# Performance work log

Hardware: AMD Instinct MI355X
Metric: run time of the kernel (lower is better)

## Reference

```python
import jax, jax.numpy as jnp
import numpy as np

HIDDEN = 1280
NUM_HEADS = 16
HEAD_DIM = HIDDEN // NUM_HEADS  # 80
ROPE_DIM = HEAD_DIM // 2        # 40
THETA = 10000.0
SEQ = 3072


def setup_inputs() -> dict:
    key = jax.random.key(0)
    ks = jax.random.split(key, 6)
    hidden_states = jax.random.normal(ks[0], (SEQ, HIDDEN), dtype=jnp.float32)
    position_ids = jax.random.randint(ks[1], (SEQ, 2), 0, 64, dtype=jnp.int32)
    qkv_w = jax.random.normal(ks[2], (HIDDEN, 3 * HIDDEN), dtype=jnp.float32) * (HIDDEN ** -0.5)
    qkv_b = jax.random.normal(ks[3], (3 * HIDDEN,), dtype=jnp.float32) * 0.02
    o_w = jax.random.normal(ks[4], (HIDDEN, HIDDEN), dtype=jnp.float32) * (HIDDEN ** -0.5)
    o_b = jax.random.normal(ks[5], (HIDDEN,), dtype=jnp.float32) * 0.02
    return {"hidden_states": hidden_states, "position_ids": position_ids,
            "qkv_w": qkv_w, "qkv_b": qkv_b, "o_w": o_w, "o_b": o_b}


def _rotate_half(x):
    x1, x2 = jnp.split(x, 2, axis=-1)
    return jnp.concatenate([-x2, x1], axis=-1)


def reference(hidden_states, position_ids, qkv_w, qkv_b, o_w, o_b):
    seq_len = hidden_states.shape[0]
    # fused QKV projection
    qkv = hidden_states @ qkv_w + qkv_b                     # (S, 3*H*D)
    qkv = qkv.reshape(seq_len, 3, NUM_HEADS, HEAD_DIM)
    q, k, v = qkv[:, 0], qkv[:, 1], qkv[:, 2]               # each (S, h, d)
    # 2D RoPE: inv_freq over rope dim = head_dim // 2
    inv_freq = 1.0 / (THETA ** (jnp.arange(0, ROPE_DIM, 2, dtype=jnp.float32) / ROPE_DIM))
    pos = position_ids.astype(jnp.float32)
    h_freqs = jnp.outer(pos[:, 0], inv_freq)                # (S, rope/2)
    w_freqs = jnp.outer(pos[:, 1], inv_freq)                # (S, rope/2)
    freqs = jnp.concatenate([h_freqs, w_freqs], axis=-1)    # (S, rope)
    emb = jnp.concatenate([freqs, freqs], axis=-1)          # (S, head_dim)
    cos = jnp.cos(emb)[:, None, :]                          # (S, 1, d)
    sin = jnp.sin(emb)[:, None, :]
    q = q * cos + _rotate_half(q) * sin
    k = k * cos + _rotate_half(k) * sin
    # manual attention
    scaling = HEAD_DIM ** -0.5
    attn = jnp.einsum('qhd,khd->hqk', q * scaling, k)       # (h, S, S)
    attn = jax.nn.softmax(attn, axis=-1)
    out = jnp.einsum('hqk,khd->qhd', attn, v)               # (S, h, d)
    out = out.reshape(seq_len, HIDDEN)
    return out @ o_w + o_b
```

## Files before the change

### kernel.cpp

```cpp
#include <hip/hip_runtime.h>

#define SEQ  3072
#define HID  1280
#define NH   16
#define HD   80
#define NQKV 3840
#define KSP  2

typedef unsigned short u16;
typedef unsigned int u32;
typedef __attribute__((ext_vector_type(8))) short short8;
typedef __attribute__((ext_vector_type(4))) short short4v;
typedef __attribute__((ext_vector_type(4))) float floatx4;

__device__ __forceinline__ u16 f2bf(float x) {
    u32 u = __float_as_uint(x);
    u += 0x7fffu + ((u >> 16) & 1u);
    return (u16)(u >> 16);
}
__device__ __forceinline__ u32 packrne(float a, float b) {
    return (u32)f2bf(a) | ((u32)f2bf(b) << 16);
}

typedef const __attribute__((address_space(1))) unsigned int* gp1_t;
typedef __attribute__((address_space(3))) unsigned int* lp3_t;
__device__ __forceinline__ void gld16(const void* g, void* l) {
    __builtin_amdgcn_global_load_lds((gp1_t)g, (lp3_t)l, 16, 0, 0);
}

__device__ __forceinline__ int swz80(int c, int r) {
    return (c < 8) ? (c ^ (r & 7)) : (8 + ((c - 8) ^ ((r >> 2) & 1)));
}

__global__ void prep_k(const int* __restrict__ pos, float* __restrict__ cosb,
                       float* __restrict__ sinb, const float* __restrict__ hs,
                       u16* __restrict__ hH, const float* __restrict__ qkvw,
                       u16* __restrict__ wT, const float* __restrict__ ow,
                       u16* __restrict__ owT) {
    __shared__ float tile[32][33];
    const int b = blockIdx.x, t = threadIdx.x;
    if (b < 480) {
        int i = b * 256 + t;
        int s = i / 40, j = i % 40;
        float p = (float)((j < 20) ? pos[s * 2] : pos[s * 2 + 1]);
        int k = (j < 20) ? j : j - 20;
        float inv = powf(10000.0f, -(float)k / 20.0f);
        float a = p * inv;
        cosb[s * 40 + j] = cosf(a);
        sinb[s * 40 + j] = sinf(a);
    } else if (b < 4320) {
        int i = (b - 480) * 256 + t;
        const float4 x = ((const float4*)hs)[i];
        uint2 o;
        o.x = packrne(x.x, x.y);
        o.y = packrne(x.z, x.w);
        ((uint2*)hH)[i] = o;
    } else {
        const float* w;
        u16* dst;
        int K, N, nx, ky;
        if (b < 9120) {
            int i = b - 4320;
            nx = i % 120; ky = i / 120; w = qkvw; dst = wT; K = HID; N = NQKV;
        } else {
            int i = b - 9120;
            nx = i % 40; ky = i / 40; w = ow; dst = owT; K = HID; N = HID;
        }
        int n0 = nx * 32, k0 = ky * 32;
        int c = t & 31, r8 = t >> 5;
        for (int rr = r8; rr < 32; rr += 8)
            tile[rr][c] = w[(size_t)(k0 + rr) * N + n0 + c];
        __syncthreads();
        for (int rr = r8; rr < 32; rr += 8)
            dst[(size_t)(n0 + rr) * K + k0 + c] = f2bf(tile[c][rr]);
    }
}

__global__ __launch_bounds__(256, 3) void gemm_bf16_k(
    const u16* __restrict__ A, const u16* __restrict__ B,
    const float* __restrict__ bias, float* __restrict__ C,
    int M, int N, int K, int mode) {
    __shared__ u16 lA[128 * 64], lB[128 * 64];
    const int t = threadIdx.x, lane = t & 63, w = t >> 6;
    const int qi = lane & 15, quad = lane >> 4;
    int id = blockIdx.x;
    int xcd = id & 7, sN = id >> 3;
    int m_idx, n_idx;
    if (mode == 0) {
        n_idx = (xcd & 1) * 15 + sN % 15;
        m_idx = (xcd >> 1) * 6 + sN / 15;
    } else {
        m_idx = xcd * 3 + sN / 10;
        n_idx = sN % 10;
    }
    const int m0 = m_idx * 128, n0 = n_idx * 128;
    const int wm = (w >> 1) * 64, wn = (w & 1) * 64;

    floatx4 acc[4][4];
    for (int mi = 0; mi < 4; mi++)
        for (int ni = 0; ni < 4; ni++) acc[mi][ni] = (floatx4){0.f, 0.f, 0.f, 0.f};

    const int rg = lane >> 3;
    const int ce = ((lane & 7) ^ rg) * 8;
    size_t gA[4], gB[4];
    for (int g = 0; g < 4; g++) {
        int row = w * 32 + g * 8 + rg;
        gA[g] = (size_t)(m0 + row) * K + ce;
        gB[g] = (size_t)(n0 + row) * K + ce;
    }

    for (int k0 = 0; k0 < K; k0 += 64) {
        for (int g = 0; g < 4; g++) {
            gld16(A + gA[g] + k0, &lA[(w * 32 + g * 8) * 64]);
            gld16(B + gB[g] + k0, &lB[(w * 32 + g * 8) * 64]);
        }
        __syncthreads();
        short8 af[4][2], bf[4][2];
        for (int mi = 0; mi < 4; mi++) {
            int row = wm + mi * 16 + qi;
            for (int kh = 0; kh < 2; kh++)
                af[mi][kh] = *(const short8*)&lA[row * 64 + (((kh * 4 + quad) ^ (row & 7)) << 3)];
        }
        for (int ni = 0; ni < 4; ni++) {
            int row = wn + ni * 16 + qi;
            for (int kh = 0; kh < 2; kh++)
                bf[ni][kh] = *(const short8*)&lB[row * 64 + (((kh * 4 + quad) ^ (row & 7)) << 3)];
        }
        for (int mi = 0; mi < 4; mi++)
            for (int ni = 0; ni < 4; ni++) {
                acc[mi][ni] = __builtin_amdgcn_mfma_f32_16x16x32_bf16(af[mi][0], bf[ni][0], acc[mi][ni], 0, 0, 0);
                acc[mi][ni] = __builtin_amdgcn_mfma_f32_16x16x32_bf16(af[mi][1], bf[ni][1], acc[mi][ni], 0, 0, 0);
            }
        __syncthreads();
    }
    for (int mi = 0; mi < 4; mi++)
        for (int ni = 0; ni < 4; ni++) {
            int col = n0 + wn + ni * 16 + qi;
            int rowb = m0 + wm + mi * 16 + quad * 4;
            float b = bias[col];
            for (int r = 0; r < 4; r++)
                C[(size_t)(rowb + r) * N + col] = acc[mi][ni][r] + b;
        }
}

__global__ void pack_qkv_k(const float* __restrict__ qkv, const float* __restrict__ cosb,
                           const float* __restrict__ sinb,
                           u16* __restrict__ Qs, u16* __restrict__ Ks, u16* __restrict__ Vs) {
    __shared__ float lv[80 * 65];
    const int t = threadIdx.x;
    const int h = blockIdx.y, s0 = blockIdx.x * 64;
    const float qsc = 0.11180339887498949f * 1.4426950408889634f;

    for (int i = t; i < 64 * 10; i += 256) {
        int rl = i / 10, jg = i % 10;
        int s = s0 + rl, j = jg * 4;
        const float4 cc = *(const float4*)&cosb[s * 40 + j];
        const float4 ss = *(const float4*)&sinb[s * 40 + j];
        const float* qb = qkv + (size_t)s * NQKV + h * HD;
        const float4 q1 = *(const float4*)&qb[j];
        const float4 q2 = *(const float4*)&qb[j + 40];
        const float* kb = qb + HID;
        const float4 k1 = *(const float4*)&kb[j];
        const float4 k2 = *(const float4*)&kb[j + 40];
        uint2 qo1, qo2, ko1, ko2;
        qo1.x = packrne((q1.x * cc.x - q2.x * ss.x) * qsc, (q1.y * cc.y - q2.y * ss.y) * qsc);
        qo1.y = packrne((q1.z * cc.z - q2.z * ss.z) * qsc, (q1.w * cc.w - q2.w * ss.w) * qsc);
        qo2.x = packrne((q2.x * cc.x + q1.x * ss.x) * qsc, (q2.y * cc.y + q1.y * ss.y) * qsc);
        qo2.y = packrne((q2.z * cc.z + q1.z * ss.z) * qsc, (q2.w * cc.w + q1.w * ss.w) * qsc);
        ko1.x = packrne(k1.x * cc.x - k2.x * ss.x, k1.y * cc.y - k2.y * ss.y);
        ko1.y = packrne(k1.z * cc.z - k2.z * ss.z, k1.w * cc.w - k2.w * ss.w);
        ko2.x = packrne(k2.x * cc.x + k1.x * ss.x, k2.y * cc.y + k1.y * ss.y);
        ko2.y = packrne(k2.z * cc.z + k1.z * ss.z, k2.w * cc.w + k1.w * ss.w);
        size_t base = (size_t)(h * SEQ + s) * 80;
        int sub0 = j & 7, sub1 = (j + 40) & 7;
        int p0 = swz80(j >> 3, s);
        int p1 = swz80((j + 40) >> 3, s);
        *(uint2*)&Qs[base + p0 * 8 + sub0] = qo1;
        *(uint2*)&Qs[base + p1 * 8 + sub1] = qo2;
        *(uint2*)&Ks[base + p0 * 8 + sub0] = ko1;
        *(uint2*)&Ks[base + p1 * 8 + sub1] = ko2;
    }
    for (int i = t; i < 64 * 80; i += 256) {
        int rl = i / 80, d = i % 80;
        lv[d * 65 + rl] = qkv[(size_t)(s0 + rl) * NQKV + 2 * HID + h * HD + d];
    }
    __syncthreads();
    for (int i = t; i < 80 * 16; i += 256) {
        int d = i / 16, g = i % 16;
        int c2l = g * 4;
        float v0 = lv[d * 65 + c2l], v1 = lv[d * 65 + c2l + 1];
        float v2 = lv[d * 65 + c2l + 2], v3 = lv[d * 65 + c2l + 3];
        int pc = (g >> 1) ^ (d & 7);
        uint2 o;
        o.x = packrne(v0, v1);
        o.y = packrne(v2, v3);
        *(uint2*)&Vs[((size_t)h * HD + d) * SEQ + s0 + pc * 8 + (g & 1) * 4] = o;
    }
}

__global__ __launch_bounds__(256, 3) void attn_k(
    const u16* __restrict__ Qs, const u16* __restrict__ Ks, const u16* __restrict__ Vs,
    float* __restrict__ Op, float* __restrict__ lp) {
    __shared__ u16 kbuf[2][5120];
    __shared__ u16 vbuf[2][5120];
    __shared__ u16 pls[4][1024];

    const int t = threadIdx.x, lane = t & 63, w = t >> 6;
    const int qi = lane & 15, quad = lane >> 4;
    const int h = blockIdx.y, q0 = blockIdx.x * 128, ksp = blockIdx.z;
    const int kc0 = ksp * (SEQ / 2);
    u16* const kflat = &kbuf[0][0];

    {
        const u16* Qt = Qs + (size_t)(h * SEQ + q0) * 80;
        for (int j = 0; j < 5; j++) {
            int o = (w * 5 + j) * 512;
            gld16(Qt + o + lane * 8, kflat + o);
        }
    }
    __syncthreads();
    short8 bq[2][3];
    for (int qg = 0; qg < 2; qg++) {
        const u16* rb = &kflat[(w * 32 + qg * 16 + qi) * 80];
        bq[qg][0] = *(const short8*)&rb[(quad ^ (qi & 7)) << 3];
        bq[qg][1] = *(const short8*)&rb[((4 + quad) ^ (qi & 7)) << 3];
        short4v t2 = *(const short4v*)&rb[((8 + ((quad >> 1) ^ ((qi >> 2) & 1))) << 3) + ((quad & 1) << 2)];
        bq[qg][2] = (short8){t2.x, t2.y, t2.z, t2.w, 0, 0, 0, 0};
    }
    __syncthreads();

    float l_lane[2] = {0.f, 0.f};
    floatx4 acco[2][5];
    for (int qg = 0; qg < 2; qg++)
        for (int dt = 0; dt < 5; dt++) acco[qg][dt] = (floatx4){0.f, 0.f, 0.f, 0.f};

    auto stage = [&](int it, int buf) {
        int kc = kc0 + it * 64;
        const u16* Kt = Ks + (size_t)(h * SEQ + kc) * 80;
        for (int i = w; i < 10; i += 4)
            gld16(Kt + i * 512 + lane * 8, &kbuf[buf][i * 512]);
        const u16* Vt = Vs + (size_t)h * HD * SEQ + kc;
        for (int i = w; i < 10; i += 4) {
            int p16 = i * 64 + lane;
            int d = p16 >> 3, pc = p16 & 7;
            gld16(Vt + (size_t)d * SEQ + pc * 8, &vbuf[buf][i * 512]);
        }
    };
    stage(0, 0);
    __syncthreads();

    const int NT = (SEQ / 2) / 64;
    char* const myp = (char*)&pls[w][0];
    for (int it = 0; it < NT; it++) {
        int cur = it & 1;
        if (it + 1 < NT) stage(it + 1, cur ^ 1);
        const u16* kb = &kbuf[cur][0];
        const u16* vb = &vbuf[cur][0];
        for (int c2 = 0; c2 < 2; c2++) {
            for (int ktl = 0; ktl < 2; ktl++) {
                int arow = (c2 * 2 + ktl) * 16 + qi;
                const u16* rb = &kb[arow * 80];
                short8 a0 = *(const short8*)&rb[(quad ^ (qi & 7)) << 3];
                short8 a1 = *(const short8*)&rb[((4 + quad) ^ (qi & 7)) << 3];
                short4v a2v = *(const short4v*)&rb[((8 + ((quad >> 1) ^ ((qi >> 2) & 1))) << 3) + ((quad & 1) << 2)];
                short8 a2 = (short8){a2v.x, a2v.y, a2v.z, a2v.w, 0, 0, 0, 0};
                for (int qg = 0; qg < 2; qg++) {
                    floatx4 s = (floatx4){0.f, 0.f, 0.f, 0.f};
                    s = __builtin_amdgcn_mfma_f32_16x16x32_bf16(a0, bq[qg][0], s, 0, 0, 0);
                    s = __builtin_amdgcn_mfma_f32_16x16x32_bf16(a1, bq[qg][1], s, 0, 0, 0);
                    s = __builtin_amdgcn_mfma_f32_16x16x32_bf16(a2, bq[qg][2], s, 0, 0, 0);
                    float e0 = __builtin_amdgcn_exp2f(s[0]);
                    float e1 = __builtin_amdgcn_exp2f(s[1]);
                    float e2 = __builtin_amdgcn_exp2f(s[2]);
                    float e3 = __builtin_amdgcn_exp2f(s[3]);
                    l_lane[qg] += (e0 + e1) + (e2 + e3);
                    uint2 pk;
                    pk.x = __builtin_amdgcn_perm(__float_as_uint(e1), __float_as_uint(e0), 0x07060302u);
                    pk.y = __builtin_amdgcn_perm(__float_as_uint(e3), __float_as_uint(e2), 0x07060302u);
                    int chunk = qg * 4 + 2 * ktl + (quad >> 1);
                    *(uint2*)(myp + qi * 128 + ((chunk ^ (qi & 7)) << 4) + ((quad & 1) << 3)) = pk;
                }
            }
            short8 bp0 = *(const short8*)(myp + qi * 128 + (((quad) ^ (qi & 7)) << 4));
            short8 bp1 = *(const short8*)(myp + qi * 128 + (((4 + quad) ^ (qi & 7)) << 4));
            int pv = (4 * c2 + quad) ^ (qi & 7);
            for (int dt = 0; dt < 5; dt++) {
                short8 av = *(const short8*)&vb[((dt * 16 + qi) * 8 + pv) * 8];
                acco[0][dt] = __builtin_amdgcn_mfma_f32_16x16x32_bf16(av, bp0, acco[0][dt], 0, 0, 0);
                acco[1][dt] = __builtin_amdgcn_mfma_f32_16x16x32_bf16(av, bp1, acco[1][dt], 0, 0, 0);
            }
        }
        __syncthreads();
    }

    for (int qg = 0; qg < 2; qg++) {
        float lq = l_lane[qg];
        lq += __shfl_xor(lq, 16);
        lq += __shfl_xor(lq, 32);
        int q = q0 + w * 32 + qg * 16 + qi;
        if (quad == 0) lp[(size_t)(ksp * NH + h) * SEQ + q] = lq;
        for (int dt = 0; dt < 5; dt++)
            for (int r = 0; r < 4; r++) {
                int d = dt * 16 + quad * 4 + r;
                Op[((size_t)(ksp * NH + h) * HD + d) * SEQ + q] = acco[qg][dt][r];
            }
    }
}

__global__ void merge_k(const float* __restrict__ Op, const float* __restrict__ lp,
                        u16* __restrict__ att) {
    __shared__ float ls[HD * 65];
    __shared__ float li[64];
    const int t = threadIdx.x;
    const int h = blockIdx.y, q0 = blockIdx.x * 64;
    for (int i = t; i < HD * 16; i += 256) {
        int d = i / 16, g = i % 16;
        size_t a0 = ((size_t)h * HD + d) * SEQ + q0 + g * 4;
        size_t a1 = ((size_t)(NH + h) * HD + d) * SEQ + q0 + g * 4;
        const float4 v0 = *(const float4*)&Op[a0];
        const float4 v1 = *(const float4*)&Op[a1];
        ls[d * 65 + g * 4 + 0] = v0.x + v1.x;
        ls[d * 65 + g * 4 + 1] = v0.y + v1.y;
        ls[d * 65 + g * 4 + 2] = v0.z + v1.z;
        ls[d * 65 + g * 4 + 3] = v0.w + v1.w;
    }
    if (t < 64)
        li[t] = 1.0f / (lp[(size_t)h * SEQ + q0 + t] + lp[(size_t)(NH + h) * SEQ + q0 + t]);
    __syncthreads();
    for (int i = t; i < 64 * 40; i += 256) {
        int ql = i / 40, dg = i % 40;
        int d0 = dg * 2;
        float s = li[ql];
        u32 o = packrne(ls[d0 * 65 + ql] * s, ls[(d0 + 1) * 65 + ql] * s);
        *(u32*)&att[(size_t)(q0 + ql) * HID + h * HD + d0] = o;
    }
}

extern "C" void kernel_launch(void* const* d_in, const int* in_sizes, int n_in,
                              void* d_out, int out_size, void* d_ws, size_t ws_size,
                              hipStream_t stream) {
    const float* hs   = (const float*)d_in[0];
    const int*   pos  = (const int*)d_in[1];
    const float* qkvw = (const float*)d_in[2];
    const float* qkvb = (const float*)d_in[3];
    const float* ow   = (const float*)d_in[4];
    const float* ob   = (const float*)d_in[5];
    float* out = (float*)d_out;

    char* p = (char*)d_ws;
    auto alloc = [&](size_t bytes) {
        char* r = p;
        p += (bytes + 255) & ~(size_t)255;
        return r;
    };
    float* cosb = (float*)alloc((size_t)SEQ * 40 * 4);
    float* sinb = (float*)alloc((size_t)SEQ * 40 * 4);
    u16* owT = (u16*)alloc((size_t)HID * HID * 2);
    char* pool1 = alloc(7864320 + 9830400);
    u16* hH = (u16*)pool1;
    u16* wT = (u16*)(pool1 + 7864320);
    u16* Qs = (u16*)pool1;
    u16* Ks = (u16*)(pool1 + 7864320);
    char* pool2 = alloc((size_t)SEQ * NQKV * 4);
    float* qkv_s = (float*)pool2;
    u16* att  = (u16*)pool2;
    float* Op = (float*)(pool2 + 7864320);
    float* lp = (float*)(pool2 + 39321600);
    u16* Vs = (u16*)alloc((size_t)NH * HD * SEQ * 2);

    hipLaunchKernelGGL(prep_k, dim3(10720), dim3(256), 0, stream,
                       pos, cosb, sinb, hs, hH, qkvw, wT, ow, owT);
    hipLaunchKernelGGL(gemm_bf16_k, dim3(720), dim3(256), 0, stream,
                       hH, wT, qkvb, qkv_s, SEQ, NQKV, HID, 0);
    hipLaunchKernelGGL(pack_qkv_k, dim3(SEQ / 64, NH), dim3(256), 0, stream,
                       qkv_s, cosb, sinb, Qs, Ks, Vs);
    hipLaunchKernelGGL(attn_k, dim3(SEQ / 128, NH, 2), dim3(256), 0, stream,
                       Qs, Ks, Vs, Op, lp);
    hipLaunchKernelGGL(merge_k, dim3(SEQ / 64, NH), dim3(256), 0, stream, Op, lp, att);
    hipLaunchKernelGGL(gemm_bf16_k, dim3(240), dim3(256), 0, stream,
                       att, owT, ob, out, SEQ, HID, HID, 1);
}
```

Before: 239.8 us.

## Replace LDS round-trip for P fragments with permlane swaps and add MFMA priority

The exponentiated attention scores were written to a per-wave LDS scratch buffer and read back in the B-operand layout for the PV MFMA. They are now kept in registers and rearranged across lanes with permlane32/permlane16 swap instructions, which removes the LDS store/load traffic and frees 8 KB of shared memory. The change also raises wave priority around MFMA sequences with s_setprio and fully unrolls the inner loops. The lane permutation must reproduce the old swizzled layout exactly, and the unrolling may raise register pressure against the 3-blocks launch bound.

```diff
diff --git a/kernel.cpp b/kernel.cpp
--- a/kernel.cpp
+++ b/kernel.cpp
@@ -12,6 +12,7 @@
 typedef __attribute__((ext_vector_type(8))) short short8;
 typedef __attribute__((ext_vector_type(4))) short short4v;
 typedef __attribute__((ext_vector_type(4))) float floatx4;
+typedef __attribute__((ext_vector_type(4))) unsigned int uint4v;
 
 __device__ __forceinline__ u16 f2bf(float x) {
     u32 u = __float_as_uint(x);
@@ -203,7 +204,6 @@
     float* __restrict__ Op, float* __restrict__ lp) {
     __shared__ u16 kbuf[2][5120];
     __shared__ u16 vbuf[2][5120];
-    __shared__ u16 pls[4][1024];
 
     const int t = threadIdx.x, lane = t & 63, w = t >> 6;
     const int qi = lane & 15, quad = lane >> 4;
@@ -250,13 +250,15 @@
     __syncthreads();
 
     const int NT = (SEQ / 2) / 64;
-    char* const myp = (char*)&pls[w][0];
     for (int it = 0; it < NT; it++) {
         int cur = it & 1;
         if (it + 1 < NT) stage(it + 1, cur ^ 1);
         const u16* kb = &kbuf[cur][0];
         const u16* vb = &vbuf[cur][0];
+#pragma unroll
         for (int c2 = 0; c2 < 2; c2++) {
+            u32 pkx[2][2], pky[2][2];
+#pragma unroll
             for (int ktl = 0; ktl < 2; ktl++) {
                 int arow = (c2 * 2 + ktl) * 16 + qi;
                 const u16* rb = &kb[arow * 80];
@@ -264,31 +266,42 @@
                 short8 a1 = *(const short8*)&rb[((4 + quad) ^ (qi & 7)) << 3];
                 short4v a2v = *(const short4v*)&rb[((8 + ((quad >> 1) ^ ((qi >> 2) & 1))) << 3) + ((quad & 1) << 2)];
                 short8 a2 = (short8){a2v.x, a2v.y, a2v.z, a2v.w, 0, 0, 0, 0};
+#pragma unroll
                 for (int qg = 0; qg < 2; qg++) {
                     floatx4 s = (floatx4){0.f, 0.f, 0.f, 0.f};
+                    __builtin_amdgcn_s_setprio(1);
                     s = __builtin_amdgcn_mfma_f32_16x16x32_bf16(a0, bq[qg][0], s, 0, 0, 0);
                     s = __builtin_amdgcn_mfma_f32_16x16x32_bf16(a1, bq[qg][1], s, 0, 0, 0);
                     s = __builtin_amdgcn_mfma_f32_16x16x32_bf16(a2, bq[qg][2], s, 0, 0, 0);
+                    __builtin_amdgcn_s_setprio(0);
                     float e0 = __builtin_amdgcn_exp2f(s[0]);
                     float e1 = __builtin_amdgcn_exp2f(s[1]);
                     float e2 = __builtin_amdgcn_exp2f(s[2]);
                     float e3 = __builtin_amdgcn_exp2f(s[3]);
                     l_lane[qg] += (e0 + e1) + (e2 + e3);
-                    uint2 pk;
-                    pk.x = __builtin_amdgcn_perm(__float_as_uint(e1), __float_as_uint(e0), 0x07060302u);
-                    pk.y = __builtin_amdgcn_perm(__float_as_uint(e3), __float_as_uint(e2), 0x07060302u);
-                    int chunk = qg * 4 + 2 * ktl + (quad >> 1);
-                    *(uint2*)(myp + qi * 128 + ((chunk ^ (qi & 7)) << 4) + ((quad & 1) << 3)) = pk;
+                    pkx[qg][ktl] = __builtin_amdgcn_perm(__float_as_uint(e1), __float_as_uint(e0), 0x07060302u);
+                    pky[qg][ktl] = __builtin_amdgcn_perm(__float_as_uint(e3), __float_as_uint(e2), 0x07060302u);
                 }
             }
-            short8 bp0 = *(const short8*)(myp + qi * 128 + (((quad) ^ (qi & 7)) << 4));
-            short8 bp1 = *(const short8*)(myp + qi * 128 + (((4 + quad) ^ (qi & 7)) << 4));
+            short8 bp[2];
+#pragma unroll
+            for (int qg = 0; qg < 2; qg++) {
+                auto s0 = __builtin_amdgcn_permlane32_swap(pkx[qg][0], pkx[qg][1], false, false);
+                auto s1 = __builtin_amdgcn_permlane32_swap(pky[qg][0], pky[qg][1], false, false);
+                auto t0 = __builtin_amdgcn_permlane16_swap(s0[0], s0[1], false, false);
+                auto t1 = __builtin_amdgcn_permlane16_swap(s1[0], s1[1], false, false);
+                uint4v bb = (uint4v){t0[0], t1[0], t0[1], t1[1]};
+                bp[qg] = __builtin_bit_cast(short8, bb);
+            }
             int pv = (4 * c2 + quad) ^ (qi & 7);
+            __builtin_amdgcn_s_setprio(1);
+#pragma unroll
             for (int dt = 0; dt < 5; dt++) {
                 short8 av = *(const short8*)&vb[((dt * 16 + qi) * 8 + pv) * 8];
-                acco[0][dt] = __builtin_amdgcn_mfma_f32_16x16x32_bf16(av, bp0, acco[0][dt], 0, 0, 0);
-                acco[1][dt] = __builtin_amdgcn_mfma_f32_16x16x32_bf16(av, bp1, acco[1][dt], 0, 0, 0);
-            }
+                acco[0][dt] = __builtin_amdgcn_mfma_f32_16x16x32_bf16(av, bp[0], acco[0][dt], 0, 0, 0);
+                acco[1][dt] = __builtin_amdgcn_mfma_f32_16x16x32_bf16(av, bp[1], acco[1][dt], 0, 0, 0);
+            }
+            __builtin_amdgcn_s_setprio(0);
         }
         __syncthreads();
     }
```

Measured after the change: 234.8 us. 1.02x faster.
